# Performance work log

Measured on AMD Instinct MI355X. Metric: run time of the kernel, lower is better.

## Reference

```python
import jax, jax.numpy as jnp
import numpy as np
import math

B, T, D = 2, 2048, 2048
H, HKV = 32, 8
DH = D // H          # 64
G = H // HKV         # 4 query heads per kv head
ROPE_BASE = 10000.0


def _rope_cos_sin(t, dh):
    inv_freq = 1.0 / (ROPE_BASE ** (jnp.arange(0, dh, 2, dtype=jnp.float32) / dh))
    pos = jnp.arange(t, dtype=jnp.float32)
    freqs = pos[:, None] * inv_freq[None, :]          # [T, Dh/2]
    emb = jnp.concatenate([freqs, freqs], axis=-1)    # [T, Dh]
    return jnp.cos(emb), jnp.sin(emb)


def _rotate_half(y):
    y1, y2 = jnp.split(y, 2, axis=-1)
    return jnp.concatenate([-y2, y1], axis=-1)


def _apply_rope(x, cos, sin):  # x: [..., T, Dh]; cos/sin: [T, Dh]
    return x * cos + _rotate_half(x) * sin


def setup_inputs() -> dict:
    key = jax.random.key(0)
    k = jax.random.split(key, 5)
    x = jax.random.normal(k[0], (B, T, D), dtype=jnp.float32)
    Wq = jax.random.normal(k[1], (D, D), dtype=jnp.float32) * 0.02
    Wk = jax.random.normal(k[2], (D, HKV * DH), dtype=jnp.float32) * 0.02
    Wv = jax.random.normal(k[3], (D, HKV * DH), dtype=jnp.float32) * 0.02
    Wo = jax.random.normal(k[4], (D, D), dtype=jnp.float32) * 0.02
    causal = jnp.tril(jnp.ones((T, T), dtype=bool))
    attn_mask = jnp.where(causal, 0.0, -1e9).astype(jnp.float32)[None, None]  # [1,1,T,T]
    return {"x": x, "Wq": Wq, "Wk": Wk, "Wv": Wv, "Wo": Wo, "attn_mask": attn_mask}


def reference(x, Wq, Wk, Wv, Wo, attn_mask):
    Bx, Tx, Dx = x.shape
    # projections (Linear, no bias)
    q = (x @ Wq).reshape(Bx, Tx, H, DH).transpose(0, 2, 1, 3)      # [B,H,T,Dh]
    kk = (x @ Wk).reshape(Bx, Tx, HKV, DH).transpose(0, 2, 1, 3)   # [B,Hkv,T,Dh]
    vv = (x @ Wv).reshape(Bx, Tx, HKV, DH).transpose(0, 2, 1, 3)   # [B,Hkv,T,Dh]
    # RoPE on q and k (offset=0, no kv cache)
    cos, sin = _rope_cos_sin(Tx, DH)
    q = _apply_rope(q, cos, sin)
    kk = _apply_rope(kk, cos, sin)
    # GQA: group query heads so head h uses kv head h // G (matches repeat_interleave)
    qg = q.reshape(Bx, HKV, G, Tx, DH)
    att = jnp.einsum('bkgtd,bksd->bkgts', qg, kk) / math.sqrt(DH)
    att = att + attn_mask[:, :, None]                              # broadcast over groups
    p = jax.nn.softmax(att, axis=-1)
    ctx = jnp.einsum('bkgts,bksd->bkgtd', p, vv)                   # [B,Hkv,G,T,Dh]
    ctx = ctx.reshape(Bx, H, Tx, DH).transpose(0, 2, 1, 3).reshape(Bx, Tx, Dx)
    return ctx @ Wo
```

## Files before the change

### kernel.cpp

```cpp
#include <hip/hip_runtime.h>
#include <hip/hip_bf16.h>


typedef __bf16 bf16_t;
typedef __bf16 bf16x4 __attribute__((ext_vector_type(4)));
typedef __bf16 bf16x8 __attribute__((ext_vector_type(8)));
typedef float f32x4 __attribute__((ext_vector_type(4)));

#define B_ 2
#define T_ 2048
#define D_ 2048
#define H_ 32
#define HKV_ 8
#define DH_ 64

__device__ __forceinline__ float fast_exp2(float x) { return __builtin_amdgcn_exp2f(x); }

__device__ __forceinline__ void gld_lds16(const bf16_t* g, bf16_t* l) {
  __builtin_amdgcn_global_load_lds((const __attribute__((address_space(1))) unsigned int*)g,
                                   (__attribute__((address_space(3))) unsigned int*)l, 16, 0, 0);
}

__global__ __launch_bounds__(256) void cast_f32_bf16(const float* __restrict__ in,
                                                     bf16_t* __restrict__ out, int n) {
  int i = (blockIdx.x * 256 + threadIdx.x) * 8;
  if (i < n) {
    f32x4 a = *(const f32x4*)&in[i];
    f32x4 b = *(const f32x4*)&in[i + 4];
    bf16x8 o;
    o[0] = (bf16_t)a[0]; o[1] = (bf16_t)a[1]; o[2] = (bf16_t)a[2]; o[3] = (bf16_t)a[3];
    o[4] = (bf16_t)b[0]; o[5] = (bf16_t)b[1]; o[6] = (bf16_t)b[2]; o[7] = (bf16_t)b[3];
    *(bf16x8*)&out[i] = o;
  }
}

__global__ __launch_bounds__(256) void transpose_w(const float* __restrict__ W,
                                                   bf16_t* __restrict__ Wt, int K, int N) {
  __shared__ float tile[64][65];
  int n0 = blockIdx.x * 64, k0 = blockIdx.y * 64;
  int tid = threadIdx.x;
  for (int i = tid; i < 4096; i += 256) {
    int r = i >> 6, c = i & 63;
    tile[r][c] = W[(size_t)(k0 + r) * N + n0 + c];
  }
  __syncthreads();
  for (int i = tid; i < 4096; i += 256) {
    int r = i >> 6, c = i & 63;
    Wt[(size_t)(n0 + r) * K + k0 + c] = (bf16_t)tile[c][r];
  }
}

template <typename OutT>
__global__ __launch_bounds__(256) void gemm_bt(const bf16_t* __restrict__ A,
                                               const bf16_t* __restrict__ Bt,
                                               OutT* __restrict__ C, int M, int N, int K) {
  __shared__ __align__(16) bf16_t As[128 * 32];
  __shared__ __align__(16) bf16_t Bs[128 * 32];
  int tid = threadIdx.x;
  int lane = tid & 63;
  int wave = tid >> 6;
  int l15 = lane & 15;
  int quad = lane >> 4;
  int m0 = blockIdx.y * 128;
  int n0 = blockIdx.x * 128;
  int wrow = (wave >> 1) * 64;
  int wcol = (wave & 1) * 64;

  f32x4 acc[4][4] = {};

  for (int kc = 0; kc < K; kc += 32) {
#pragma unroll
    for (int c = 0; c < 2; ++c) {
      int linear = c * 256 + tid;
      int r = linear >> 2, seg = linear & 3;
      gld_lds16(&A[(size_t)(m0 + r) * K + kc + seg * 8],
                &As[(size_t)(c * 256 + wave * 64) * 8]);
      gld_lds16(&Bt[(size_t)(n0 + r) * K + kc + seg * 8],
                &Bs[(size_t)(c * 256 + wave * 64) * 8]);
    }
    __syncthreads();
    bf16x8 af[4], bfr[4];
#pragma unroll
    for (int mi = 0; mi < 4; ++mi)
      af[mi] = *(const bf16x8*)&As[(wrow + mi * 16 + l15) * 32 + quad * 8];
#pragma unroll
    for (int ni = 0; ni < 4; ++ni)
      bfr[ni] = *(const bf16x8*)&Bs[(wcol + ni * 16 + l15) * 32 + quad * 8];
#pragma unroll
    for (int mi = 0; mi < 4; ++mi)
#pragma unroll
      for (int ni = 0; ni < 4; ++ni)
        acc[mi][ni] = __builtin_amdgcn_mfma_f32_16x16x32_bf16(af[mi], bfr[ni], acc[mi][ni], 0, 0, 0);
    __syncthreads();
  }
#pragma unroll
  for (int mi = 0; mi < 4; ++mi) {
#pragma unroll
    for (int ni = 0; ni < 4; ++ni) {
#pragma unroll
      for (int r = 0; r < 4; ++r) {
        int m = m0 + wrow + mi * 16 + quad * 4 + r;
        int n = n0 + wcol + ni * 16 + l15;
        C[(size_t)m * N + n] = (OutT)acc[mi][ni][r];
      }
    }
  }
}

__global__ __launch_bounds__(256) void rope_qk(const bf16_t* __restrict__ qkv,
                                               bf16_t* __restrict__ qr,
                                               bf16_t* __restrict__ kr) {
  int t = blockIdx.x, b = blockIdx.y;
  int tid = threadIdx.x;
  const bf16_t* row = qkv + (size_t)(b * T_ + t) * 3072;
  const float LN1E4_over32 = 9.210340371976184f / 32.0f;
  for (int i = tid; i < 1024 + 256; i += 256) {
    bool isq = i < 1024;
    int ii = isq ? i : i - 1024;
    int hh = ii >> 5, j = ii & 31;
    int base = isq ? 0 : 2048;
    float inv = __expf(-(float)j * LN1E4_over32);
    float fr = (float)t * inv;
    float sn, cs;
    sincosf(fr, &sn, &cs);
    float x1 = (float)row[base + hh * 64 + j];
    float x2 = (float)row[base + hh * 64 + j + 32];
    float o1 = x1 * cs - x2 * sn;
    float o2 = x2 * cs + x1 * sn;
    if (isq) {
      size_t o = ((size_t)(b * H_ + hh) * T_ + t) * DH_;
      qr[o + j] = (bf16_t)o1;
      qr[o + j + 32] = (bf16_t)o2;
    } else {
      size_t o = ((size_t)(b * HKV_ + hh) * T_ + t) * DH_;
      kr[o + j] = (bf16_t)o1;
      kr[o + j + 32] = (bf16_t)o2;
    }
  }
}

__global__ __launch_bounds__(256) void transpose_v(const bf16_t* __restrict__ qkv,
                                                   bf16_t* __restrict__ vtr) {
  __shared__ __align__(16) bf16_t tile[64][72];
  int t0 = blockIdx.x * 64;
  int hk = blockIdx.y;
  int b = blockIdx.z;
  int tid = threadIdx.x;
  for (int i = tid; i < 512; i += 256) {
    int r = i >> 3, s = i & 7;
    *(bf16x8*)&tile[r][s * 8] =
        *(const bf16x8*)&qkv[(size_t)(b * T_ + t0 + r) * 3072 + 2560 + hk * 64 + s * 8];
  }
  __syncthreads();
  for (int i = tid; i < 4096; i += 256) {
    int dd = i >> 6, tt = i & 63;
    vtr[((size_t)(b * HKV_ + hk) * DH_ + dd) * T_ + t0 + tt] = tile[tt][dd];
  }
}

#define DO_HALF(HALF, QF, O, LACC, DOMASK)                                             \
  {                                                                                    \
    f32x4 s_[4] = {};                                                                  \
    _Pragma("unroll") for (int mt = 0; mt < 4; ++mt) {                                 \
      bf16x8 ak0 = *(const bf16x8*)&Ks[(mt * 16 + l15) * 72 + quad * 8];               \
      bf16x8 ak1 = *(const bf16x8*)&Ks[(mt * 16 + l15) * 72 + 32 + quad * 8];          \
      s_[mt] = __builtin_amdgcn_mfma_f32_16x16x32_bf16(ak0, QF[0], s_[mt], 0, 0, 0);   \
      s_[mt] = __builtin_amdgcn_mfma_f32_16x16x32_bf16(ak1, QF[1], s_[mt], 0, 0, 0);   \
    }                                                                                  \
    if (DOMASK) {                                                                      \
      _Pragma("unroll") for (int mt = 0; mt < 4; ++mt)                                 \
          _Pragma("unroll") for (int r = 0; r < 4; ++r) if (mt * 16 + quad * 4 + r >   \
                                                            wave * 16 + l15)           \
              s_[mt][r] = -1e30f;                                                      \
    }                                                                                  \
    _Pragma("unroll") for (int mt = 0; mt < 4; ++mt) {                                 \
      bf16x4 pv;                                                                       \
      _Pragma("unroll") for (int r = 0; r < 4; ++r) {                                  \
        float p = fast_exp2(s_[mt][r] * CS);                                           \
        LACC += p;                                                                     \
        pv[r] = (bf16_t)p;                                                             \
      }                                                                                \
      *(bf16x4*)&Ps[wave][HALF][l15 * 72 + mt * 16 + quad * 4] = pv;                   \
    }                                                                                  \
    _Pragma("unroll") for (int k0 = 0; k0 < 2; ++k0) {                                 \
      bf16x8 ap = *(const bf16x8*)&Ps[wave][HALF][l15 * 72 + k0 * 32 + quad * 8];      \
      _Pragma("unroll") for (int dn = 0; dn < 4; ++dn) {                               \
        bf16x8 bv = *(const bf16x8*)&Vt[(dn * 16 + l15) * 72 + k0 * 32 + quad * 8];    \
        O[dn] = __builtin_amdgcn_mfma_f32_16x16x32_bf16(ap, bv, O[dn], 0, 0, 0);       \
      }                                                                                \
    }                                                                                  \
  }

__global__ __launch_bounds__(256) void flash_attn(const bf16_t* __restrict__ qr,
                                                  const bf16_t* __restrict__ kr,
                                                  const bf16_t* __restrict__ vtr,
                                                  bf16_t* __restrict__ ctxb) {
  __shared__ __align__(16) bf16_t Ks[64 * 72];
  __shared__ __align__(16) bf16_t Vt[64 * 72];
  __shared__ __align__(16) bf16_t Ps[4][2][16 * 72];
  int tid = threadIdx.x;
  int lane = tid & 63;
  int wave = tid >> 6;
  int l15 = lane & 15, quad = lane >> 4;
  int pair = blockIdx.x, h = blockIdx.y, b = blockIdx.z;
  int qtA = pair, qtB = 31 - pair;
  int nkvA = qtA + 1, nkvB = qtB + 1;
  int kvh = h >> 2;
  const float CS = 1.44269504088896f * 0.125f;

  const bf16_t* qbA = qr + ((size_t)(b * H_ + h) * T_ + qtA * 64 + wave * 16) * DH_;
  const bf16_t* qbB = qr + ((size_t)(b * H_ + h) * T_ + qtB * 64 + wave * 16) * DH_;
  const bf16_t* kbase = kr + (size_t)(b * HKV_ + kvh) * T_ * DH_;
  const bf16_t* vbase = vtr + (size_t)(b * HKV_ + kvh) * DH_ * T_;

  bf16x8 qA[2], qB[2];
#pragma unroll
  for (int k0 = 0; k0 < 2; ++k0) {
    qA[k0] = *(const bf16x8*)&qbA[l15 * 64 + k0 * 32 + quad * 8];
    qB[k0] = *(const bf16x8*)&qbB[l15 * 64 + k0 * 32 + quad * 8];
  }

  f32x4 oA[4] = {}, oB[4] = {};
  float lA = 0.f, lB = 0.f;

  bf16x8 kreg[2], vreg[2];
  auto load_kv = [&](int kv) {
#pragma unroll
    for (int c = 0; c < 2; ++c) {
      int idx = c * 256 + tid;
      int r = idx >> 3, sg = idx & 7;
      kreg[c] = *(const bf16x8*)&kbase[(size_t)kv * 4096 + r * 64 + sg * 8];
      vreg[c] = *(const bf16x8*)&vbase[(size_t)r * T_ + kv * 64 + sg * 8];
    }
  };
  load_kv(0);

  for (int kv = 0; kv < nkvB; ++kv) {
#pragma unroll
    for (int c = 0; c < 2; ++c) {
      int idx = c * 256 + tid;
      int r = idx >> 3, sg = idx & 7;
      *(bf16x8*)&Ks[r * 72 + sg * 8] = kreg[c];
      *(bf16x8*)&Vt[r * 72 + sg * 8] = vreg[c];
    }
    __syncthreads();
    if (kv + 1 < nkvB) load_kv(kv + 1);

    DO_HALF(1, qB, oB, lB, kv == qtB);
    if (kv < nkvA) DO_HALF(0, qA, oA, lA, kv == qtA);
    __syncthreads();
  }

  lA += __shfl_xor(lA, 16, 64);
  lA += __shfl_xor(lA, 32, 64);
  lB += __shfl_xor(lB, 16, 64);
  lB += __shfl_xor(lB, 32, 64);
  float invA = 1.0f / lA, invB = 1.0f / lB;
#pragma unroll
  for (int r = 0; r < 4; ++r) {
    float iAr = __shfl(invA, quad * 4 + r, 64);
    float iBr = __shfl(invB, quad * 4 + r, 64);
    int tA = qtA * 64 + wave * 16 + quad * 4 + r;
    int tB = qtB * 64 + wave * 16 + quad * 4 + r;
#pragma unroll
    for (int dn = 0; dn < 4; ++dn) {
      ctxb[(size_t)(b * T_ + tA) * D_ + h * 64 + dn * 16 + l15] = (bf16_t)(oA[dn][r] * iAr);
      ctxb[(size_t)(b * T_ + tB) * D_ + h * 64 + dn * 16 + l15] = (bf16_t)(oB[dn][r] * iBr);
    }
  }
}

extern "C" void kernel_launch(void* const* d_in, const int* in_sizes, int n_in,
                              void* d_out, int out_size, void* d_ws, size_t ws_size,
                              hipStream_t stream) {
  const float* x = (const float*)d_in[0];
  const float* Wq = (const float*)d_in[1];
  const float* Wk = (const float*)d_in[2];
  const float* Wv = (const float*)d_in[3];
  const float* Wo = (const float*)d_in[4];
  float* out = (float*)d_out;

  char* ws = (char*)d_ws;
  size_t off = 0;
  bf16_t* xb = (bf16_t*)(ws + off); off += (size_t)B_ * T_ * D_ * 2;
  bf16_t* wqkvb = (bf16_t*)(ws + off); off += (size_t)3072 * 2048 * 2;
  bf16_t* wob = (bf16_t*)(ws + off); off += (size_t)2048 * 2048 * 2;
  bf16_t* qkv = (bf16_t*)(ws + off); off += (size_t)4096 * 3072 * 2;
  bf16_t* qr = (bf16_t*)(ws + off); off += (size_t)B_ * H_ * T_ * DH_ * 2;
  bf16_t* kr = (bf16_t*)(ws + off); off += (size_t)B_ * HKV_ * T_ * DH_ * 2;
  bf16_t* vtr = (bf16_t*)(ws + off); off += (size_t)B_ * HKV_ * T_ * DH_ * 2;
  bf16_t* ctxb = (bf16_t*)(ws + off); off += (size_t)B_ * T_ * D_ * 2;

  int nx = B_ * T_ * D_;
  cast_f32_bf16<<<nx / 8 / 256, 256, 0, stream>>>(x, xb, nx);
  transpose_w<<<dim3(2048 / 64, 2048 / 64), 256, 0, stream>>>(Wq, wqkvb, 2048, 2048);
  transpose_w<<<dim3(512 / 64, 2048 / 64), 256, 0, stream>>>(Wk, wqkvb + (size_t)2048 * 2048, 2048, 512);
  transpose_w<<<dim3(512 / 64, 2048 / 64), 256, 0, stream>>>(Wv, wqkvb + (size_t)2560 * 2048, 2048, 512);
  transpose_w<<<dim3(2048 / 64, 2048 / 64), 256, 0, stream>>>(Wo, wob, 2048, 2048);

  gemm_bt<bf16_t><<<dim3(3072 / 128, 4096 / 128), 256, 0, stream>>>(xb, wqkvb, qkv, 4096, 3072, 2048);

  rope_qk<<<dim3(T_, B_), 256, 0, stream>>>(qkv, qr, kr);
  transpose_v<<<dim3(T_ / 64, HKV_, B_), 256, 0, stream>>>(qkv, vtr);

  flash_attn<<<dim3(16, H_, B_), 256, 0, stream>>>(qr, kr, vtr, ctxb);

  gemm_bt<float><<<dim3(2048 / 128, 4096 / 128), 256, 0, stream>>>(ctxb, wob, out, 4096, 2048, 2048);
}
```

Baseline: 362.5 us.

## Fuse QKV weight transposes, deepen GEMM K-step, fold softmax scale into Q

Merges the three Q/K/V weight-transpose launches into a single kernel that picks its source matrix by column block. The GEMM now loads two 32-wide K slices per iteration, which halves the number of barrier pairs per K sweep at the cost of doubling LDS use per block. The softmax scale (log2e/sqrt(dh)) is applied to Q during RoPE, which removes a multiply per score in the attention inner loop. Q is therefore rounded to bf16 after scaling, which slightly changes rounding.

```diff
diff --git a/kernel.cpp b/kernel.cpp
--- a/kernel.cpp
+++ b/kernel.cpp
@@ -50,12 +50,35 @@
   }
 }
 
+__global__ __launch_bounds__(256) void transpose_wqkv(const float* __restrict__ Wq,
+                                                      const float* __restrict__ Wk,
+                                                      const float* __restrict__ Wv,
+                                                      bf16_t* __restrict__ Wt) {
+  __shared__ float tile[64][65];
+  int n0 = blockIdx.x * 64, k0 = blockIdx.y * 64;
+  const float* W;
+  int srcN, col;
+  if (n0 < 2048) { W = Wq; srcN = 2048; col = n0; }
+  else if (n0 < 2560) { W = Wk; srcN = 512; col = n0 - 2048; }
+  else { W = Wv; srcN = 512; col = n0 - 2560; }
+  int tid = threadIdx.x;
+  for (int i = tid; i < 4096; i += 256) {
+    int r = i >> 6, c = i & 63;
+    tile[r][c] = W[(size_t)(k0 + r) * srcN + col + c];
+  }
+  __syncthreads();
+  for (int i = tid; i < 4096; i += 256) {
+    int r = i >> 6, c = i & 63;
+    Wt[(size_t)(n0 + r) * 2048 + k0 + c] = (bf16_t)tile[c][r];
+  }
+}
+
 template <typename OutT>
 __global__ __launch_bounds__(256) void gemm_bt(const bf16_t* __restrict__ A,
                                                const bf16_t* __restrict__ Bt,
                                                OutT* __restrict__ C, int M, int N, int K) {
-  __shared__ __align__(16) bf16_t As[128 * 32];
-  __shared__ __align__(16) bf16_t Bs[128 * 32];
+  __shared__ __align__(16) bf16_t As[2 * 128 * 32];
+  __shared__ __align__(16) bf16_t Bs[2 * 128 * 32];
   int tid = threadIdx.x;
   int lane = tid & 63;
   int wave = tid >> 6;
@@ -68,29 +91,35 @@
 
   f32x4 acc[4][4] = {};
 
-  for (int kc = 0; kc < K; kc += 32) {
-#pragma unroll
-    for (int c = 0; c < 2; ++c) {
-      int linear = c * 256 + tid;
-      int r = linear >> 2, seg = linear & 3;
-      gld_lds16(&A[(size_t)(m0 + r) * K + kc + seg * 8],
-                &As[(size_t)(c * 256 + wave * 64) * 8]);
-      gld_lds16(&Bt[(size_t)(n0 + r) * K + kc + seg * 8],
-                &Bs[(size_t)(c * 256 + wave * 64) * 8]);
+  for (int kc = 0; kc < K; kc += 64) {
+#pragma unroll
+    for (int kk = 0; kk < 2; ++kk) {
+#pragma unroll
+      for (int c = 0; c < 2; ++c) {
+        int linear = c * 256 + tid;
+        int r = linear >> 2, seg = linear & 3;
+        gld_lds16(&A[(size_t)(m0 + r) * K + kc + kk * 32 + seg * 8],
+                  &As[kk * 4096 + (size_t)(c * 256 + wave * 64) * 8]);
+        gld_lds16(&Bt[(size_t)(n0 + r) * K + kc + kk * 32 + seg * 8],
+                  &Bs[kk * 4096 + (size_t)(c * 256 + wave * 64) * 8]);
+      }
     }
     __syncthreads();
-    bf16x8 af[4], bfr[4];
-#pragma unroll
-    for (int mi = 0; mi < 4; ++mi)
-      af[mi] = *(const bf16x8*)&As[(wrow + mi * 16 + l15) * 32 + quad * 8];
-#pragma unroll
-    for (int ni = 0; ni < 4; ++ni)
-      bfr[ni] = *(const bf16x8*)&Bs[(wcol + ni * 16 + l15) * 32 + quad * 8];
-#pragma unroll
-    for (int mi = 0; mi < 4; ++mi)
+#pragma unroll
+    for (int kk = 0; kk < 2; ++kk) {
+      bf16x8 af[4], bfr[4];
+#pragma unroll
+      for (int mi = 0; mi < 4; ++mi)
+        af[mi] = *(const bf16x8*)&As[kk * 4096 + (wrow + mi * 16 + l15) * 32 + quad * 8];
 #pragma unroll
       for (int ni = 0; ni < 4; ++ni)
-        acc[mi][ni] = __builtin_amdgcn_mfma_f32_16x16x32_bf16(af[mi], bfr[ni], acc[mi][ni], 0, 0, 0);
+        bfr[ni] = *(const bf16x8*)&Bs[kk * 4096 + (wcol + ni * 16 + l15) * 32 + quad * 8];
+#pragma unroll
+      for (int mi = 0; mi < 4; ++mi)
+#pragma unroll
+        for (int ni = 0; ni < 4; ++ni)
+          acc[mi][ni] = __builtin_amdgcn_mfma_f32_16x16x32_bf16(af[mi], bfr[ni], acc[mi][ni], 0, 0, 0);
+    }
     __syncthreads();
   }
 #pragma unroll
@@ -114,6 +143,7 @@
   int tid = threadIdx.x;
   const bf16_t* row = qkv + (size_t)(b * T_ + t) * 3072;
   const float LN1E4_over32 = 9.210340371976184f / 32.0f;
+  const float QSC = 1.44269504088896f * 0.125f;
   for (int i = tid; i < 1024 + 256; i += 256) {
     bool isq = i < 1024;
     int ii = isq ? i : i - 1024;
@@ -129,8 +159,8 @@
     float o2 = x2 * cs + x1 * sn;
     if (isq) {
       size_t o = ((size_t)(b * H_ + hh) * T_ + t) * DH_;
-      qr[o + j] = (bf16_t)o1;
-      qr[o + j + 32] = (bf16_t)o2;
+      qr[o + j] = (bf16_t)(o1 * QSC);
+      qr[o + j + 32] = (bf16_t)(o2 * QSC);
     } else {
       size_t o = ((size_t)(b * HKV_ + hh) * T_ + t) * DH_;
       kr[o + j] = (bf16_t)o1;
@@ -176,7 +206,7 @@
     _Pragma("unroll") for (int mt = 0; mt < 4; ++mt) {                                 \
       bf16x4 pv;                                                                       \
       _Pragma("unroll") for (int r = 0; r < 4; ++r) {                                  \
-        float p = fast_exp2(s_[mt][r] * CS);                                           \
+        float p = fast_exp2(s_[mt][r]);                                                \
         LACC += p;                                                                     \
         pv[r] = (bf16_t)p;                                                             \
       }                                                                                \
@@ -206,7 +236,6 @@
   int qtA = pair, qtB = 31 - pair;
   int nkvA = qtA + 1, nkvB = qtB + 1;
   int kvh = h >> 2;
-  const float CS = 1.44269504088896f * 0.125f;
 
   const bf16_t* qbA = qr + ((size_t)(b * H_ + h) * T_ + qtA * 64 + wave * 16) * DH_;
   const bf16_t* qbB = qr + ((size_t)(b * H_ + h) * T_ + qtB * 64 + wave * 16) * DH_;
@@ -293,9 +322,7 @@
 
   int nx = B_ * T_ * D_;
   cast_f32_bf16<<<nx / 8 / 256, 256, 0, stream>>>(x, xb, nx);
-  transpose_w<<<dim3(2048 / 64, 2048 / 64), 256, 0, stream>>>(Wq, wqkvb, 2048, 2048);
-  transpose_w<<<dim3(512 / 64, 2048 / 64), 256, 0, stream>>>(Wk, wqkvb + (size_t)2048 * 2048, 2048, 512);
-  transpose_w<<<dim3(512 / 64, 2048 / 64), 256, 0, stream>>>(Wv, wqkvb + (size_t)2560 * 2048, 2048, 512);
+  transpose_wqkv<<<dim3(3072 / 64, 2048 / 64), 256, 0, stream>>>(Wq, Wk, Wv, wqkvb);
   transpose_w<<<dim3(2048 / 64, 2048 / 64), 256, 0, stream>>>(Wo, wob, 2048, 2048);
 
   gemm_bt<bf16_t><<<dim3(3072 / 128, 4096 / 128), 256, 0, stream>>>(xb, wqkvb, qkv, 4096, 3072, 2048);
```

After: 329.2 us. 9.2% less time.
